# Kernel tuning notes

Hardware: AMD Instinct MI355X
Metric: run time of the kernel (lower is better)

The kernel has to match this reference:

```python
import jax, jax.numpy as jnp
import numpy as np

B, D, T = 8192, 1024, 3          # batch, input_dim, num_tasks
E, HM, OM = 8, 2048, 512         # mmoe: experts, hidden, output
P, S, HC, OC = 3, 4, 1024, 256   # ple: specific, shared, hidden, output
TH, OUT = 256, 1                 # tower hidden, out_dim per task
EPS = 1e-5


def _ln(h):
    mu = jnp.mean(h, axis=-1, keepdims=True)
    v = jnp.mean((h - mu) ** 2, axis=-1, keepdims=True)
    return (h - mu) * jax.lax.rsqrt(v + EPS)


def setup_inputs() -> dict:
    key = jax.random.key(0)
    ks = iter(jax.random.split(key, 64))
    def w(*shape):
        return 0.02 * jax.random.normal(next(ks), shape, jnp.float32)
    z = lambda *s: jnp.zeros(s, jnp.float32)
    o = lambda *s: jnp.ones(s, jnp.float32)
    return {
        "x": jax.random.normal(next(ks), (B, D), jnp.float32),
        "mmoe_w1": w(E, D, HM), "mmoe_b1": z(E, HM), "mmoe_g": o(E, HM), "mmoe_be": z(E, HM),
        "mmoe_w2": w(E, HM, OM), "mmoe_b2": z(E, OM),
        "mmoe_gw": w(T, D, E), "mmoe_gb": z(T, E),
        "c0_sw1": w(S, OM, HC), "c0_sb1": z(S, HC), "c0_sg": o(S, HC), "c0_sbe": z(S, HC),
        "c0_sw2": w(S, HC, OC), "c0_sb2": z(S, OC),
        "c0_tw1": w(T, P, OM, HC), "c0_tb1": z(T, P, HC), "c0_tg": o(T, P, HC), "c0_tbe": z(T, P, HC),
        "c0_tw2": w(T, P, HC, OC), "c0_tb2": z(T, P, OC),
        "c0_gw": w(T, OM, P + S), "c0_gb": z(T, P + S),
        "c0_sgw": w(OM, T * P + S), "c0_sgb": z(T * P + S),
        "c1_sw1": w(S, OC, HC), "c1_sb1": z(S, HC), "c1_sg": o(S, HC), "c1_sbe": z(S, HC),
        "c1_sw2": w(S, HC, OC), "c1_sb2": z(S, OC),
        "c1_tw1": w(T, P, OC, HC), "c1_tb1": z(T, P, HC), "c1_tg": o(T, P, HC), "c1_tbe": z(T, P, HC),
        "c1_tw2": w(T, P, HC, OC), "c1_tb2": z(T, P, OC),
        "c1_gw": w(T, OC, P + S), "c1_gb": z(T, P + S),
        "tow_w1": w(T, OC, TH), "tow_b1": z(T, TH), "tow_w2": w(T, TH, OUT), "tow_b2": z(T, OUT),
    }


def _cgc(shared_in, task_in, sw1, sb1, sg, sbe, sw2, sb2,
         tw1, tb1, tg, tbe, tw2, tb2, gw, gb, sgw=None, sgb=None):
    # shared experts: [S, B, O]
    hs = jnp.einsum('bd,sdh->sbh', shared_in, sw1) + sb1[:, None, :]
    hs = jax.nn.relu(_ln(hs) * sg[:, None, :] + sbe[:, None, :])
    so = jnp.einsum('sbh,sho->sbo', hs, sw2) + sb2[:, None, :]
    # task-specific experts: [T, P, B, O]
    ht = jnp.einsum('tbd,tpdh->tpbh', task_in, tw1) + tb1[:, :, None, :]
    ht = jax.nn.relu(_ln(ht) * tg[:, :, None, :] + tbe[:, :, None, :])
    to = jnp.einsum('tpbh,tpho->tpbo', ht, tw2) + tb2[:, :, None, :]
    Tn, Pn, Bn, On = to.shape
    Sn = so.shape[0]
    # per-task expert bank: task-specific first, then shared (matches torch.cat order)
    ex = jnp.concatenate([to, jnp.broadcast_to(so[None], (Tn, Sn, Bn, On))], axis=1)
    gate = jax.nn.softmax(jnp.einsum('tbd,tde->tbe', task_in, gw) + gb[:, None, :], axis=-1)
    task_out = jnp.einsum('tbe,tebo->tbo', gate, ex)
    if sgw is None:
        return None, task_out
    all_ex = jnp.concatenate([to.reshape(Tn * Pn, Bn, On), so], axis=0)
    sgate = jax.nn.softmax(shared_in @ sgw + sgb, axis=-1)
    shared_out = jnp.einsum('be,ebo->bo', sgate, all_ex)
    return shared_out, task_out


def _fwd(x, mmoe_w1, mmoe_b1, mmoe_g, mmoe_be, mmoe_w2, mmoe_b2, mmoe_gw, mmoe_gb,
         c0_sw1, c0_sb1, c0_sg, c0_sbe, c0_sw2, c0_sb2,
         c0_tw1, c0_tb1, c0_tg, c0_tbe, c0_tw2, c0_tb2, c0_gw, c0_gb, c0_sgw, c0_sgb,
         c1_sw1, c1_sb1, c1_sg, c1_sbe, c1_sw2, c1_sb2,
         c1_tw1, c1_tb1, c1_tg, c1_tbe, c1_tw2, c1_tb2, c1_gw, c1_gb,
         tow_w1, tow_b1, tow_w2, tow_b2):
    # --- MMoE layer (dropout = identity in eval) ---
    h = jnp.einsum('bd,edh->ebh', x, mmoe_w1) + mmoe_b1[:, None, :]
    h = jax.nn.relu(_ln(h) * mmoe_g[:, None, :] + mmoe_be[:, None, :])
    eo = jnp.einsum('ebh,eho->ebo', h, mmoe_w2) + mmoe_b2[:, None, :]  # [E,B,OM]
    gate = jax.nn.softmax(jnp.einsum('bd,tde->tbe', x, mmoe_gw) + mmoe_gb[:, None, :], axis=-1)
    task_hs = jnp.einsum('tbe,ebo->tbo', gate, eo)  # [T,B,OM]
    shared_h = jnp.mean(task_hs, axis=0)            # 'mean' aggregate
    # --- PLE CGC layers ---
    shared_h, task_hs = _cgc(shared_h, task_hs, c0_sw1, c0_sb1, c0_sg, c0_sbe, c0_sw2, c0_sb2,
                             c0_tw1, c0_tb1, c0_tg, c0_tbe, c0_tw2, c0_tb2, c0_gw, c0_gb, c0_sgw, c0_sgb)
    _, task_hs = _cgc(shared_h, task_hs, c1_sw1, c1_sb1, c1_sg, c1_sbe, c1_sw2, c1_sb2,
                      c1_tw1, c1_tb1, c1_tg, c1_tbe, c1_tw2, c1_tb2, c1_gw, c1_gb)
    # --- task towers ---
    th = jax.nn.relu(jnp.einsum('tbo,toh->tbh', task_hs, tow_w1) + tow_b1[:, None, :])
    return jnp.einsum('tbh,tho->tbo', th, tow_w2) + tow_b2[:, None, :]  # [T,B,OUT]


def reference(x, mmoe_w1, mmoe_b1, mmoe_g, mmoe_be, mmoe_w2, mmoe_b2, mmoe_gw, mmoe_gb,
              c0_sw1, c0_sb1, c0_sg, c0_sbe, c0_sw2, c0_sb2,
              c0_tw1, c0_tb1, c0_tg, c0_tbe, c0_tw2, c0_tb2, c0_gw, c0_gb, c0_sgw, c0_sgb,
              c1_sw1, c1_sb1, c1_sg, c1_sbe, c1_sw2, c1_sb2,
              c1_tw1, c1_tb1, c1_tg, c1_tbe, c1_tw2, c1_tb2, c1_gw, c1_gb,
              tow_w1, tow_b1, tow_w2, tow_b2):
    return _fwd(x, mmoe_w1, mmoe_b1, mmoe_g, mmoe_be, mmoe_w2, mmoe_b2, mmoe_gw, mmoe_gb,
                c0_sw1, c0_sb1, c0_sg, c0_sbe, c0_sw2, c0_sb2,
                c0_tw1, c0_tb1, c0_tg, c0_tbe, c0_tw2, c0_tb2, c0_gw, c0_gb, c0_sgw, c0_sgb,
                c1_sw1, c1_sb1, c1_sg, c1_sbe, c1_sw2, c1_sb2,
                c1_tw1, c1_tb1, c1_tg, c1_tbe, c1_tw2, c1_tb2, c1_gw, c1_gb,
                tow_w1, tow_b1, tow_w2, tow_b2)
```

## Files before the change

### kernel.cpp

```cpp
#include <hip/hip_runtime.h>

typedef unsigned short u16;
typedef unsigned int   u32;
typedef __bf16  bf16x8 __attribute__((ext_vector_type(8)));
typedef float   f32x4  __attribute__((ext_vector_type(4)));

#define B_ 8192
#define DI __device__ __forceinline__

DI u16 f2bf(float f) {
  u32 u = __float_as_uint(f);
  u = (u + 0x7fffu + ((u >> 16) & 1u)) >> 16;
  return (u16)u;
}
DI float bf2f(u16 h) { return __uint_as_float(((u32)h) << 16); }

DI void gll(const u16* g, u16* l) {
  __builtin_amdgcn_global_load_lds(
      (const __attribute__((address_space(1))) void*)g,
      (__attribute__((address_space(3))) void*)l, 16, 0, 0);
}

__global__ __launch_bounds__(256) void transpose_cast(
    const float* __restrict__ W, u16* __restrict__ Wt, int K, int N) {
  __shared__ float tile[64][65];
  int g = blockIdx.z;
  int k0 = blockIdx.x * 64, n0 = blockIdx.y * 64;
  const float* Wg = W + (size_t)g * K * N;
  u16* Og = Wt + (size_t)g * N * K;
  int tid = threadIdx.x;
  int rr = tid >> 4, cc = (tid & 15) * 4;
#pragma unroll
  for (int r = 0; r < 4; ++r) {
    int k = rr + r * 16;
    float4 v = *(const float4*)(Wg + (size_t)(k0 + k) * N + n0 + cc);
    tile[k][cc] = v.x; tile[k][cc + 1] = v.y; tile[k][cc + 2] = v.z; tile[k][cc + 3] = v.w;
  }
  __syncthreads();
  int nr = tid >> 3, kc = (tid & 7) * 8;
#pragma unroll
  for (int p = 0; p < 2; ++p) {
    int n = nr + p * 32;
    u16 tmp[8];
#pragma unroll
    for (int j = 0; j < 8; ++j) tmp[j] = f2bf(tile[kc + j][n]);
    *(uint4*)(Og + (size_t)(n0 + n) * K + k0 + kc) = *(uint4*)tmp;
  }
}

__global__ __launch_bounds__(256) void cast_bf16k(const float* __restrict__ X, u16* __restrict__ Y) {
  size_t i = ((size_t)blockIdx.x * 256 + threadIdx.x) * 4;
  float4 v = *(const float4*)(X + i);
  u16 t[4] = { f2bf(v.x), f2bf(v.y), f2bf(v.z), f2bf(v.w) };
  *(uint2*)(Y + i) = *(uint2*)t;
}

#define BM 128
#define BK 32
#define LDK 32

template<int BN_>
__global__ __launch_bounds__(256) void gemm_t(
    const u16* __restrict__ A, long a_stride, int a_div, int a_g0,
    const u16* __restrict__ Wt, const float* __restrict__ bias,
    u16* __restrict__ C, long c_stride, int N, int K, int relu_flag) {
  constexpr int JT = BN_ / 32;
  constexpr int BROWS = BN_ / 4;
  int gz = blockIdx.z;
  const u16* Ag = A + (size_t)((a_g0 + gz) / a_div) * a_stride;
  const u16* Wg = Wt + (size_t)gz * N * K;
  u16* Cg = C + (size_t)gz * c_stride;
  int m0 = blockIdx.x * BM, n0 = blockIdx.y * BN_;

  __shared__ __align__(16) u16 As[BM * LDK];
  __shared__ __align__(16) u16 Bs[BN_ * LDK];

  int tid = threadIdx.x;
  int wv = tid >> 6, ln = tid & 63;
  int wm = (wv >> 1) * 64, wn = (wv & 1) * (BN_ / 2);
  int lr = ln & 15, lk = (ln >> 4) * 8;

  int sr = ln >> 2;
  int sc = (ln & 3) * 8;
  const u16* aG = Ag + (size_t)(m0 + wv * 32 + sr) * K + sc;
  const u16* bG = Wg + (size_t)(n0 + wv * BROWS + sr) * K + sc;
  u16* aL0 = As + (wv * 32) * LDK;
  u16* aL1 = aL0 + 16 * LDK;
  u16* bL0 = Bs + (wv * BROWS) * LDK;

  f32x4 acc[4][JT];
#pragma unroll
  for (int i = 0; i < 4; ++i)
#pragma unroll
    for (int j = 0; j < JT; ++j)
      acc[i][j] = (f32x4){0.f, 0.f, 0.f, 0.f};

  int nk = K / BK;
  for (int ks = 0; ks < nk; ++ks) {
    __syncthreads();
    gll(aG + ks * BK, aL0);
    gll(aG + ks * BK + (size_t)16 * K, aL1);
    gll(bG + ks * BK, bL0);
    if (BN_ == 128) gll(bG + ks * BK + (size_t)16 * K, bL0 + 16 * LDK);
    __syncthreads();
    bf16x8 af[4], bfr[JT];
#pragma unroll
    for (int i = 0; i < 4; ++i) {
      union { uint4 u; bf16x8 v; } ua;
      ua.u = *(const uint4*)(As + (wm + i * 16 + lr) * LDK + lk);
      af[i] = ua.v;
    }
#pragma unroll
    for (int j = 0; j < JT; ++j) {
      union { uint4 u; bf16x8 v; } ub;
      ub.u = *(const uint4*)(Bs + (wn + j * 16 + lr) * LDK + lk);
      bfr[j] = ub.v;
    }
#pragma unroll
    for (int i = 0; i < 4; ++i)
#pragma unroll
      for (int j = 0; j < JT; ++j)
        acc[i][j] = __builtin_amdgcn_mfma_f32_16x16x32_bf16(af[i], bfr[j], acc[i][j], 0, 0, 0);
  }

  int mr = (ln >> 4) * 4;
#pragma unroll
  for (int i = 0; i < 4; ++i) {
#pragma unroll
    for (int j = 0; j < JT; ++j) {
      int n = n0 + wn + j * 16 + lr;
      float bv = bias[(size_t)gz * N + n];
#pragma unroll
      for (int r = 0; r < 4; ++r) {
        int m = m0 + wm + i * 16 + mr + r;
        float v = acc[i][j][r] + bv;
        if (relu_flag) v = fmaxf(v, 0.f);
        Cg[(size_t)m * N + n] = f2bf(v);
      }
    }
  }
}

__global__ __launch_bounds__(256) void ln_affine_relu(
    u16* __restrict__ H, const float* __restrict__ gain, const float* __restrict__ beta,
    int N, int rows_per_group) {
  __shared__ float red[4];
  size_t row = blockIdx.x;
  int grp = (int)(row / (size_t)rows_per_group);
  u16* hp = H + row * N;
  const float* gp = gain + (size_t)grp * N;
  const float* bp = beta + (size_t)grp * N;
  int tid = threadIdx.x;
  int nw = blockDim.x >> 6;
  union { uint4 u; u16 s[8]; } pk;
  pk.u = *(const uint4*)(hp + tid * 8);
  float v[8], s = 0.f;
#pragma unroll
  for (int j = 0; j < 8; ++j) { v[j] = bf2f(pk.s[j]); s += v[j]; }
  for (int off = 32; off > 0; off >>= 1) s += __shfl_down(s, off, 64);
  if ((tid & 63) == 0) red[tid >> 6] = s;
  __syncthreads();
  float tot = 0.f;
  for (int i = 0; i < nw; ++i) tot += red[i];
  float mu = tot / (float)N;
  float q = 0.f;
#pragma unroll
  for (int j = 0; j < 8; ++j) { float d = v[j] - mu; q += d * d; }
  __syncthreads();
  for (int off = 32; off > 0; off >>= 1) q += __shfl_down(q, off, 64);
  if ((tid & 63) == 0) red[tid >> 6] = q;
  __syncthreads();
  tot = 0.f;
  for (int i = 0; i < nw; ++i) tot += red[i];
  float rstd = rsqrtf(tot / (float)N + 1e-5f);
  float4 ga = *(const float4*)(gp + tid * 8);
  float4 gb2 = *(const float4*)(gp + tid * 8 + 4);
  float4 ba = *(const float4*)(bp + tid * 8);
  float4 bb2 = *(const float4*)(bp + tid * 8 + 4);
  float gg[8] = { ga.x, ga.y, ga.z, ga.w, gb2.x, gb2.y, gb2.z, gb2.w };
  float bt[8] = { ba.x, ba.y, ba.z, ba.w, bb2.x, bb2.y, bb2.z, bb2.w };
  u16 o[8];
#pragma unroll
  for (int j = 0; j < 8; ++j) {
    float y = (v[j] - mu) * rstd * gg[j] + bt[j];
    o[j] = f2bf(fmaxf(y, 0.f));
  }
  *(uint4*)(hp + tid * 8) = *(uint4*)o;
}

__global__ __launch_bounds__(256) void prep_gw4(
    const float* __restrict__ W, float* __restrict__ out4,
    int G, int K, int E, int L) {
  int id = blockIdx.x * 256 + threadIdx.x;
  int tot = (K >> 2) * 32;
  if (id >= tot) return;
  int k4 = id >> 5, j = id & 31;
  int t = j / L, e = j % L;
  float4 v = { 0.f, 0.f, 0.f, 0.f };
  if (t < G && e < E) {
    const float* w = W + (size_t)t * K * E + e;
    v.x = w[(size_t)(k4 * 4 + 0) * E];
    v.y = w[(size_t)(k4 * 4 + 1) * E];
    v.z = w[(size_t)(k4 * 4 + 2) * E];
    v.w = w[(size_t)(k4 * 4 + 3) * E];
  }
  *(float4*)(out4 + (size_t)id * 4) = v;
}

__global__ __launch_bounds__(256) void gates_fast(
    const void* __restrict__ X, int is_bf16, long t_stride,
    const float* __restrict__ GW4, const float* __restrict__ GB,
    float* __restrict__ out, int G, int K, int E, int L) {
  int tid = threadIdx.x;
  int rl = tid >> 5;
  int j  = tid & 31;
  int t = j / L, e = j % L;
  int b = blockIdx.x * 8 + rl;
  int tr = (t < G) ? t : (G - 1);
  int K4 = K >> 2;
  float ac[8];
#pragma unroll
  for (int u = 0; u < 8; ++u) ac[u] = 0.f;
  if (is_bf16) {
    const u16* xr = (const u16*)X + (size_t)tr * t_stride + (size_t)b * K;
    for (int k4 = 0; k4 < K4; k4 += 8) {
      uint2 p[8]; float4 q[8];
#pragma unroll
      for (int u = 0; u < 8; ++u) {
        p[u] = *(const uint2*)(xr + (k4 + u) * 4);
        q[u] = *(const float4*)(GW4 + ((size_t)(k4 + u) * 32 + j) * 4);
      }
#pragma unroll
      for (int u = 0; u < 8; ++u)
        ac[u] += bf2f((u16)(p[u].x & 0xffffu)) * q[u].x + bf2f((u16)(p[u].x >> 16)) * q[u].y
               + bf2f((u16)(p[u].y & 0xffffu)) * q[u].z + bf2f((u16)(p[u].y >> 16)) * q[u].w;
    }
  } else {
    const float* xr = (const float*)X + (size_t)tr * t_stride + (size_t)b * K;
    for (int k4 = 0; k4 < K4; k4 += 8) {
      float4 xv[8]; float4 q[8];
#pragma unroll
      for (int u = 0; u < 8; ++u) {
        xv[u] = *(const float4*)(xr + (k4 + u) * 4);
        q[u] = *(const float4*)(GW4 + ((size_t)(k4 + u) * 32 + j) * 4);
      }
#pragma unroll
      for (int u = 0; u < 8; ++u)
        ac[u] += xv[u].x * q[u].x + xv[u].y * q[u].y + xv[u].z * q[u].z + xv[u].w * q[u].w;
    }
  }
  float acc = ((ac[0] + ac[1]) + (ac[2] + ac[3])) + ((ac[4] + ac[5]) + (ac[6] + ac[7]));
  bool valid = (t < G) && (e < E);
  float lg = valid ? (acc + GB[t * E + e]) : -1e30f;
  float m = lg;
  for (int o = L >> 1; o > 0; o >>= 1) m = fmaxf(m, __shfl_xor(m, o, L));
  float ex = valid ? expf(lg - m) : 0.f;
  float sm = ex;
  for (int o = L >> 1; o > 0; o >>= 1) sm += __shfl_xor(sm, o, L);
  if (valid) out[((size_t)t * B_ + b) * E + e] = ex / sm;
}

__global__ __launch_bounds__(256) void mmoe_mix(
    const u16* __restrict__ eo, const float* __restrict__ gates,
    u16* __restrict__ task_hs, u16* __restrict__ shared_h) {
  __shared__ float g[24];
  int b = blockIdx.x, tid = threadIdx.x;
  if (tid < 24) g[tid] = gates[((size_t)(tid >> 3) * B_ + b) * 8 + (tid & 7)];
  __syncthreads();
  int o = tid * 2;
  float a0[3] = {0, 0, 0}, a1[3] = {0, 0, 0};
#pragma unroll
  for (int e = 0; e < 8; ++e) {
    u32 w = *(const u32*)(eo + ((size_t)e * B_ + b) * 512 + o);
    float v0 = bf2f((u16)(w & 0xffffu)), v1 = bf2f((u16)(w >> 16));
#pragma unroll
    for (int t = 0; t < 3; ++t) { a0[t] += g[t * 8 + e] * v0; a1[t] += g[t * 8 + e] * v1; }
  }
  float s0 = 0.f, s1 = 0.f;
#pragma unroll
  for (int t = 0; t < 3; ++t) {
    u16 p[2] = { f2bf(a0[t]), f2bf(a1[t]) };
    *(u32*)(task_hs + ((size_t)t * B_ + b) * 512 + o) = *(u32*)p;
    s0 += a0[t]; s1 += a1[t];
  }
  u16 p[2] = { f2bf(s0 * (1.f / 3.f)), f2bf(s1 * (1.f / 3.f)) };
  *(u32*)(shared_h + (size_t)b * 512 + o) = *(u32*)p;
}

__global__ __launch_bounds__(256) void cgc_mix(
    const u16* __restrict__ to, const u16* __restrict__ so,
    const float* __restrict__ g, const float* __restrict__ sg,
    u16* __restrict__ task_out, u16* __restrict__ shared_out) {
  int b = blockIdx.x, o = threadIdx.x;
  float tv[9], sv[4];
#pragma unroll
  for (int j = 0; j < 9; ++j) tv[j] = bf2f(to[((size_t)j * B_ + b) * 256 + o]);
#pragma unroll
  for (int s = 0; s < 4; ++s) sv[s] = bf2f(so[((size_t)s * B_ + b) * 256 + o]);
#pragma unroll
  for (int t = 0; t < 3; ++t) {
    const float* gt = g + ((size_t)t * B_ + b) * 7;
    float a = gt[0] * tv[t * 3] + gt[1] * tv[t * 3 + 1] + gt[2] * tv[t * 3 + 2];
#pragma unroll
    for (int s = 0; s < 4; ++s) a += gt[3 + s] * sv[s];
    task_out[((size_t)t * B_ + b) * 256 + o] = f2bf(a);
  }
  if (shared_out) {
    const float* sp = sg + (size_t)b * 13;
    float a = 0.f;
#pragma unroll
    for (int j = 0; j < 9; ++j) a += sp[j] * tv[j];
#pragma unroll
    for (int s = 0; s < 4; ++s) a += sp[9 + s] * sv[s];
    shared_out[(size_t)b * 256 + o] = f2bf(a);
  }
}

__global__ __launch_bounds__(256) void tower_out(
    const u16* __restrict__ th, const float* __restrict__ w2,
    const float* __restrict__ b2, float* __restrict__ out) {
  int r = blockIdx.x * 4 + (threadIdx.x >> 6);
  int lane = threadIdx.x & 63;
  int t = r / B_;
  const u16* row = th + (size_t)r * 256;
  u16 hv[4];
  *(uint2*)hv = *(const uint2*)(row + lane * 4);
  float4 wv = *(const float4*)(w2 + t * 256 + lane * 4);
  float s = bf2f(hv[0]) * wv.x + bf2f(hv[1]) * wv.y + bf2f(hv[2]) * wv.z + bf2f(hv[3]) * wv.w;
  for (int off = 32; off > 0; off >>= 1) s += __shfl_down(s, off, 64);
  if (lane == 0) out[r] = s + b2[t];
}

extern "C" void kernel_launch(void* const* d_in, const int* in_sizes, int n_in,
                              void* d_out, int out_size, void* d_ws, size_t ws_size,
                              hipStream_t stream) {
  (void)in_sizes; (void)n_in; (void)out_size;
  const float* x      = (const float*)d_in[0];
  const float* m_w1   = (const float*)d_in[1];
  const float* m_b1   = (const float*)d_in[2];
  const float* m_g    = (const float*)d_in[3];
  const float* m_be   = (const float*)d_in[4];
  const float* m_w2   = (const float*)d_in[5];
  const float* m_b2   = (const float*)d_in[6];
  const float* m_gw   = (const float*)d_in[7];
  const float* m_gb   = (const float*)d_in[8];
  const float* c0_sw1 = (const float*)d_in[9];
  const float* c0_sb1 = (const float*)d_in[10];
  const float* c0_sg  = (const float*)d_in[11];
  const float* c0_sbe = (const float*)d_in[12];
  const float* c0_sw2 = (const float*)d_in[13];
  const float* c0_sb2 = (const float*)d_in[14];
  const float* c0_tw1 = (const float*)d_in[15];
  const float* c0_tb1 = (const float*)d_in[16];
  const float* c0_tg  = (const float*)d_in[17];
  const float* c0_tbe = (const float*)d_in[18];
  const float* c0_tw2 = (const float*)d_in[19];
  const float* c0_tb2 = (const float*)d_in[20];
  const float* c0_gw  = (const float*)d_in[21];
  const float* c0_gb  = (const float*)d_in[22];
  const float* c0_sgw = (const float*)d_in[23];
  const float* c0_sgb = (const float*)d_in[24];
  const float* c1_sw1 = (const float*)d_in[25];
  const float* c1_sb1 = (const float*)d_in[26];
  const float* c1_sg  = (const float*)d_in[27];
  const float* c1_sbe = (const float*)d_in[28];
  const float* c1_sw2 = (const float*)d_in[29];
  const float* c1_sb2 = (const float*)d_in[30];
  const float* c1_tw1 = (const float*)d_in[31];
  const float* c1_tb1 = (const float*)d_in[32];
  const float* c1_tg  = (const float*)d_in[33];
  const float* c1_tbe = (const float*)d_in[34];
  const float* c1_tw2 = (const float*)d_in[35];
  const float* c1_tb2 = (const float*)d_in[36];
  const float* c1_gw  = (const float*)d_in[37];
  const float* c1_gb  = (const float*)d_in[38];
  const float* tw1    = (const float*)d_in[39];
  const float* tb1    = (const float*)d_in[40];
  const float* tw2    = (const float*)d_in[41];
  const float* tb2    = (const float*)d_in[42];

  const size_t MB = 1024 * 1024;
  char* ws = (char*)d_ws;
  if (ws_size < 163 * MB) return;
  u16* XB      = (u16*)(ws);
  u16* W1T     = (u16*)(ws + 16 * MB);
  u16* W2T     = (u16*)(ws + 48 * MB);
  u16* HID     = (u16*)(ws + 64 * MB);
  u16* EO      = (u16*)(ws + 96 * MB);
  u16* TASK_HS = (u16*)(ws + 16 * MB);
  u16* SHARED_H= (u16*)(ws + 40 * MB);
  u16* SO0     = (u16*)(ws);
  u16* C0_SW1T = (u16*)(ws + 48 * MB);
  u16* C0_SW2T = (u16*)(ws + 52 * MB);
  u16* C0_TW1T = (u16*)(ws + 54 * MB);
  u16* C0_TW2T = (u16*)(ws + 63 * MB);
  u16* HID0    = (u16*)(ws + 68 * MB);
  u16* TO0     = (u16*)(ws + 104 * MB);
  u16* TASK1   = (u16*)(ws + 16 * MB);
  u16* SHARED1 = (u16*)(ws + 28 * MB);
  u16* SO1     = (u16*)(ws);
  u16* C1_SW1T = (u16*)(ws + 48 * MB);
  u16* C1_SW2T = (u16*)(ws + 50 * MB);
  u16* C1_TW1T = (u16*)(ws + 52 * MB);
  u16* C1_TW2T = (u16*)(ws + 56 * MB + 512 * 1024);
  u16* HID1    = (u16*)(ws + 68 * MB);
  u16* TO1     = (u16*)(ws + 104 * MB);
  u16* TASK2   = (u16*)(ws + 32 * MB);
  u16* TWT     = (u16*)(ws + 48 * MB);
  u16* TH      = (u16*)(ws + 104 * MB);

  float* gbase = (float*)(ws + 160 * MB);
  float* gmo  = gbase;
  float* g0   = gmo  + (size_t)3 * B_ * 8;
  float* sg0  = g0   + (size_t)3 * B_ * 7;
  float* g1   = sg0  + (size_t)B_ * 13;
  float* gw4a = g1   + (size_t)3 * B_ * 7;
  float* gw4b = gw4a + 32768;

  dim3 blk(256);
  cast_bf16k<<<8192, blk, 0, stream>>>(x, XB);

  prep_gw4<<<32, blk, 0, stream>>>(m_gw, gw4a, 3, 1024, 8, 8);
  gates_fast<<<B_ / 8, blk, 0, stream>>>(x, 0, 0L, gw4a, m_gb, gmo, 3, 1024, 8, 8);

  transpose_cast<<<dim3(16, 32, 8), blk, 0, stream>>>(m_w1, W1T, 1024, 2048);
  transpose_cast<<<dim3(32,  8, 8), blk, 0, stream>>>(m_w2, W2T, 2048, 512);
  for (int c = 0; c < 8; ++c) {
    size_t r0 = (size_t)c * 1024;
    gemm_t<128><<<dim3(8, 16, 8), blk, 0, stream>>>(
        XB + r0 * 1024, 0L, 1, 0, W1T, m_b1, HID, (long)1024 * 2048, 2048, 1024, 0);
    ln_affine_relu<<<8 * 1024, 256, 0, stream>>>(HID, m_g, m_be, 2048, 1024);
    gemm_t<64><<<dim3(8, 8, 8), blk, 0, stream>>>(
        HID, (long)1024 * 2048, 1, 0, W2T, m_b2, EO + r0 * 512, (long)B_ * 512, 512, 2048, 0);
  }
  mmoe_mix<<<B_, blk, 0, stream>>>(EO, gmo, TASK_HS, SHARED_H);

  prep_gw4<<<16, blk, 0, stream>>>(c0_gw, gw4a, 3, 512, 7, 8);
  prep_gw4<<<16, blk, 0, stream>>>(c0_sgw, gw4b, 1, 512, 13, 16);
  gates_fast<<<B_ / 8, blk, 0, stream>>>(TASK_HS, 1, (long)B_ * 512, gw4a, c0_gb, g0, 3, 512, 7, 8);
  gates_fast<<<B_ / 8, blk, 0, stream>>>(SHARED_H, 1, 0L, gw4b, c0_sgb, sg0, 1, 512, 13, 16);

  transpose_cast<<<dim3( 8, 16, 4), blk, 0, stream>>>(c0_sw1, C0_SW1T, 512, 1024);
  transpose_cast<<<dim3(16,  4, 4), blk, 0, stream>>>(c0_sw2, C0_SW2T, 1024, 256);
  transpose_cast<<<dim3( 8, 16, 9), blk, 0, stream>>>(c0_tw1, C0_TW1T, 512, 1024);
  transpose_cast<<<dim3(16,  4, 9), blk, 0, stream>>>(c0_tw2, C0_TW2T, 1024, 256);
  for (int c = 0; c < 2; ++c) {
    size_t r0 = (size_t)c * 4096;
    gemm_t<128><<<dim3(32, 8, 4), blk, 0, stream>>>(
        SHARED_H + r0 * 512, 0L, 1, 0, C0_SW1T, c0_sb1, HID0, (long)4096 * 1024, 1024, 512, 0);
    ln_affine_relu<<<4 * 4096, 128, 0, stream>>>(HID0, c0_sg, c0_sbe, 1024, 4096);
    gemm_t<64><<<dim3(32, 4, 4), blk, 0, stream>>>(
        HID0, (long)4096 * 1024, 1, 0, C0_SW2T, c0_sb2, SO0 + r0 * 256, (long)B_ * 256, 256, 1024, 0);
  }
  for (int c = 0; c < 4; ++c) {
    size_t r0 = (size_t)c * 2048;
    gemm_t<128><<<dim3(16, 8, 9), blk, 0, stream>>>(
        TASK_HS + r0 * 512, (long)B_ * 512, 3, 0, C0_TW1T, c0_tb1, HID0, (long)2048 * 1024, 1024, 512, 0);
    ln_affine_relu<<<9 * 2048, 128, 0, stream>>>(HID0, c0_tg, c0_tbe, 1024, 2048);
    gemm_t<64><<<dim3(16, 4, 9), blk, 0, stream>>>(
        HID0, (long)2048 * 1024, 1, 0, C0_TW2T, c0_tb2, TO0 + r0 * 256, (long)B_ * 256, 256, 1024, 0);
  }
  cgc_mix<<<B_, blk, 0, stream>>>(TO0, SO0, g0, sg0, TASK1, SHARED1);

  prep_gw4<<<8, blk, 0, stream>>>(c1_gw, gw4a, 3, 256, 7, 8);
  gates_fast<<<B_ / 8, blk, 0, stream>>>(TASK1, 1, (long)B_ * 256, gw4a, c1_gb, g1, 3, 256, 7, 8);

  transpose_cast<<<dim3( 4, 16, 4), blk, 0, stream>>>(c1_sw1, C1_SW1T, 256, 1024);
  transpose_cast<<<dim3(16,  4, 4), blk, 0, stream>>>(c1_sw2, C1_SW2T, 1024, 256);
  transpose_cast<<<dim3( 4, 16, 9), blk, 0, stream>>>(c1_tw1, C1_TW1T, 256, 1024);
  transpose_cast<<<dim3(16,  4, 9), blk, 0, stream>>>(c1_tw2, C1_TW2T, 1024, 256);
  for (int c = 0; c < 2; ++c) {
    size_t r0 = (size_t)c * 4096;
    gemm_t<128><<<dim3(32, 8, 4), blk, 0, stream>>>(
        SHARED1 + r0 * 256, 0L, 1, 0, C1_SW1T, c1_sb1, HID1, (long)4096 * 1024, 1024, 256, 0);
    ln_affine_relu<<<4 * 4096, 128, 0, stream>>>(HID1, c1_sg, c1_sbe, 1024, 4096);
    gemm_t<64><<<dim3(32, 4, 4), blk, 0, stream>>>(
        HID1, (long)4096 * 1024, 1, 0, C1_SW2T, c1_sb2, SO1 + r0 * 256, (long)B_ * 256, 256, 1024, 0);
  }
  for (int c = 0; c < 4; ++c) {
    size_t r0 = (size_t)c * 2048;
    gemm_t<128><<<dim3(16, 8, 9), blk, 0, stream>>>(
        TASK1 + r0 * 256, (long)B_ * 256, 3, 0, C1_TW1T, c1_tb1, HID1, (long)2048 * 1024, 1024, 256, 0);
    ln_affine_relu<<<9 * 2048, 128, 0, stream>>>(HID1, c1_tg, c1_tbe, 1024, 2048);
    gemm_t<64><<<dim3(16, 4, 9), blk, 0, stream>>>(
        HID1, (long)2048 * 1024, 1, 0, C1_TW2T, c1_tb2, TO1 + r0 * 256, (long)B_ * 256, 256, 1024, 0);
  }
  cgc_mix<<<B_, blk, 0, stream>>>(TO1, SO1, g1, nullptr, TASK2, nullptr);

  transpose_cast<<<dim3(4, 4, 3), blk, 0, stream>>>(tw1, TWT, 256, 256);
  gemm_t<64><<<dim3(64, 4, 3), blk, 0, stream>>>(
      TASK2, (long)B_ * 256, 1, 0, TWT, tb1, TH, (long)B_ * 256, 256, 256, 1);
  tower_out<<<6144, blk, 0, stream>>>(TH, tw2, tb2, (float*)d_out);
}
```

Measured before the change: 2.247 ms.

## Double-buffer GEMM LDS tiles and XOR-swizzle K chunks to avoid bank conflicts

The bf16 MFMA GEMM kernel now uses two LDS buffers for the A and B tiles. It issues the global-to-LDS loads for the next K step before computing on the current one, so load latency overlaps with the MFMAs and there is one barrier per step instead of two. The 8-element K chunks are also XOR-swizzled by row, consistently on store and load, to reduce LDS bank conflicts on the fragment reads. This doubles shared memory per block, which may lower occupancy. The loop assumes K/BK is even.

```diff
diff --git a/kernel.cpp b/kernel.cpp
--- a/kernel.cpp
+++ b/kernel.cpp
@@ -72,21 +72,23 @@
   u16* Cg = C + (size_t)gz * c_stride;
   int m0 = blockIdx.x * BM, n0 = blockIdx.y * BN_;
 
-  __shared__ __align__(16) u16 As[BM * LDK];
-  __shared__ __align__(16) u16 Bs[BN_ * LDK];
+  __shared__ __align__(16) u16 As0[BM * LDK];
+  __shared__ __align__(16) u16 As1[BM * LDK];
+  __shared__ __align__(16) u16 Bs0[BN_ * LDK];
+  __shared__ __align__(16) u16 Bs1[BN_ * LDK];
 
   int tid = threadIdx.x;
   int wv = tid >> 6, ln = tid & 63;
   int wm = (wv >> 1) * 64, wn = (wv & 1) * (BN_ / 2);
-  int lr = ln & 15, lk = (ln >> 4) * 8;
+  int lr = ln & 15;
+  int lk = ((ln >> 4) ^ ((ln >> 1) & 3)) * 8;
 
   int sr = ln >> 2;
-  int sc = (ln & 3) * 8;
+  int sc = (((ln & 3) ^ ((ln >> 3) & 3))) * 8;
   const u16* aG = Ag + (size_t)(m0 + wv * 32 + sr) * K + sc;
   const u16* bG = Wg + (size_t)(n0 + wv * BROWS + sr) * K + sc;
-  u16* aL0 = As + (wv * 32) * LDK;
-  u16* aL1 = aL0 + 16 * LDK;
-  u16* bL0 = Bs + (wv * BROWS) * LDK;
+  const int aOff = (wv * 32) * LDK;
+  const int bOff = (wv * BROWS) * LDK;
 
   f32x4 acc[4][JT];
 #pragma unroll
@@ -95,14 +97,15 @@
     for (int j = 0; j < JT; ++j)
       acc[i][j] = (f32x4){0.f, 0.f, 0.f, 0.f};
 
-  int nk = K / BK;
-  for (int ks = 0; ks < nk; ++ks) {
-    __syncthreads();
-    gll(aG + ks * BK, aL0);
-    gll(aG + ks * BK + (size_t)16 * K, aL1);
-    gll(bG + ks * BK, bL0);
-    if (BN_ == 128) gll(bG + ks * BK + (size_t)16 * K, bL0 + 16 * LDK);
-    __syncthreads();
+  auto stage = [&](u16* As, u16* Bs, int ks) {
+    const u16* aP = aG + ks * BK;
+    const u16* bP = bG + ks * BK;
+    gll(aP, As + aOff);
+    gll(aP + (size_t)16 * K, As + aOff + 16 * LDK);
+    gll(bP, Bs + bOff);
+    if (BN_ == 128) gll(bP + (size_t)16 * K, Bs + bOff + 16 * LDK);
+  };
+  auto compute = [&](const u16* As, const u16* Bs) {
     bf16x8 af[4], bfr[JT];
 #pragma unroll
     for (int i = 0; i < 4; ++i) {
@@ -121,6 +124,18 @@
 #pragma unroll
       for (int j = 0; j < JT; ++j)
         acc[i][j] = __builtin_amdgcn_mfma_f32_16x16x32_bf16(af[i], bfr[j], acc[i][j], 0, 0, 0);
+  };
+
+  int nk = K / BK;
+  stage(As0, Bs0, 0);
+  __syncthreads();
+  for (int ks = 0; ks < nk; ks += 2) {
+    stage(As1, Bs1, ks + 1);
+    compute(As0, Bs0);
+    __syncthreads();
+    if (ks + 2 < nk) stage(As0, Bs0, ks + 2);
+    compute(As1, Bs1);
+    __syncthreads();
   }
 
   int mr = (ln >> 4) * 4;
```

Measured after the change: 2.099 ms. 6.6% less time.
